# Kernel optimization log

Measured on AMD Instinct MI355X. Metric: run time of the kernel, lower is better.

Reference implementation:

```python
import jax, jax.numpy as jnp
import numpy as np

K = 128      # num_states
V = 50257    # vocab_size
D = 128      # tag_emb_dim
H = 128      # trans_hidden_dim
B = 64       # batch
T = 2048     # seq len


def setup_inputs() -> dict:
    key = jax.random.key(0)
    ks = jax.random.split(key, 6)
    s = 0.02
    return {
        "batch_emissions": jax.random.randint(ks[0], (B, T), 0, V, dtype=jnp.int32),
        "init_logits": jnp.zeros((K,), jnp.float32),
        "tag_embed": (jax.random.normal(ks[1], (K, D)) * s).astype(jnp.float32),
        "word_embed": (jax.random.normal(ks[2], (V, D)) * s).astype(jnp.float32),
        "word_bias": jnp.zeros((V,), jnp.float32),
        "trans_query": (jax.random.normal(ks[3], (H,)) * s).astype(jnp.float32),
        "trans_W": (jax.random.normal(ks[4], (K * K, H)) * s).astype(jnp.float32),
        "trans_b": jnp.zeros((K * K,), jnp.float32),
    }


def reference(batch_emissions, init_logits, tag_embed, word_embed, word_bias,
              trans_query, trans_W, trans_b):
    # log initial probs (K,)
    log_pi = jax.nn.log_softmax(init_logits)
    # log transition probs (K, K): row i = p(z_t | z_{t-1}=i)
    log_A = jax.nn.log_softmax((trans_W @ trans_query + trans_b).reshape(K, K), axis=1)
    # log emission probs (K, V)
    log_Bm = jax.nn.log_softmax(tag_embed @ word_embed.T + word_bias[None, :], axis=1)
    # gather per-token emissions: (B, T, K)
    emit = log_Bm.T[batch_emissions]

    alpha0 = log_pi[None, :] + emit[:, 0]  # (B, K)

    def step(alpha, e_t):
        # alpha: (B, K) over prev state i; log-semiring matvec with log_A
        a = jax.scipy.special.logsumexp(alpha[:, :, None] + log_A[None, :, :], axis=1) + e_t
        return a, None

    emit_rest = jnp.swapaxes(emit[:, 1:], 0, 1)  # (T-1, B, K)
    alpha_T, _ = jax.lax.scan(step, alpha0, emit_rest)

    log_likelihood = jax.scipy.special.logsumexp(alpha_T, axis=-1)  # (B,)
    return -jnp.sum(log_likelihood)
```

## Files before the change

### kernel.cpp

```cpp
#include <hip/hip_runtime.h>


#define KK 128
#define TT 2048
#define BB 64

typedef int v8i __attribute__((ext_vector_type(8)));
typedef float v4f __attribute__((ext_vector_type(4)));

__device__ __forceinline__ float wave_sum64(float v) {
#pragma unroll
  for (int m = 32; m; m >>= 1) v += __shfl_xor(v, m, 64);
  return v;
}
__device__ __forceinline__ float wave_max64(float v) {
#pragma unroll
  for (int m = 32; m; m >>= 1) v = fmaxf(v, __shfl_xor(v, m, 64));
  return v;
}
__device__ __forceinline__ unsigned short f2bf(float x) {
  union { float f; unsigned u; } c; c.f = x;
  unsigned r = c.u + 0x7fffu + ((c.u >> 16) & 1u);
  return (unsigned short)(r >> 16);
}
__device__ __forceinline__ float bflo(unsigned u) {
  union { unsigned u; float f; } c; c.u = u << 16; return c.f;
}
__device__ __forceinline__ float bfhi(unsigned u) {
  union { unsigned u; float f; } c; c.u = u & 0xffff0000u; return c.f;
}

__device__ __forceinline__ float fp8dec_sw(unsigned byte) {
  unsigned em = byte & 0x7fu;
  float v;
  if (em < 8) {
    v = (float)em * 0x1p-9f;
  } else {
    union { unsigned u; float f; } x;
    x.u = (em << 20) + (120u << 23);
    v = x.f;
  }
  return (byte & 0x80u) ? -v : v;
}

__global__ __launch_bounds__(128, 1)
void k_emis(const float* __restrict__ tag, const float* __restrict__ word,
            const float* __restrict__ bias, unsigned short* __restrict__ E128,
            float* __restrict__ partialZ, int V) {
  __shared__ float4 wtile[128 * 32];
  __shared__ float btile[128];
  const int tid = threadIdx.x;
  const int v0 = blockIdx.x * 128;

  const float4* w4 = (const float4*)word;
  const int maxi = V * 32 - 1;
#pragma unroll
  for (int it = 0; it < 32; ++it) {
    int idx = it * 128 + tid;
    int g = v0 * 32 + idx;
    wtile[idx] = w4[min(g, maxi)];
  }
  btile[tid] = (v0 + tid < V) ? bias[v0 + tid] : 0.f;

  float treg[128];
  const float4* t4 = (const float4*)(tag + (size_t)tid * 128);
#pragma unroll
  for (int c = 0; c < 32; ++c) {
    float4 x = t4[c];
    treg[4 * c + 0] = x.x; treg[4 * c + 1] = x.y;
    treg[4 * c + 2] = x.z; treg[4 * c + 3] = x.w;
  }
  __syncthreads();

  float zp = 0.f;
  for (int v = 0; v < 128; ++v) {
    if (v0 + v >= V) break;
    const float4* row = &wtile[v * 32];
    float a0 = 0.f, a1 = 0.f, a2 = 0.f, a3 = 0.f;
#pragma unroll
    for (int c = 0; c < 32; ++c) {
      float4 pv = row[c];
      a0 = fmaf(pv.x, treg[4 * c + 0], a0);
      a1 = fmaf(pv.y, treg[4 * c + 1], a1);
      a2 = fmaf(pv.z, treg[4 * c + 2], a2);
      a3 = fmaf(pv.w, treg[4 * c + 3], a3);
    }
    float e = __expf((a0 + a1) + (a2 + a3) + btile[v]);
    E128[(size_t)(v0 + v) * KK + tid] = f2bf(128.f * e);
    zp += e;
  }
  partialZ[(size_t)blockIdx.x * KK + tid] = zp;
}

__global__ __launch_bounds__(128)
void k_trans(const float* __restrict__ W, const float* __restrict__ q,
             const float* __restrict__ tb, const float* __restrict__ pZ,
             const float* __restrict__ initlog, float* __restrict__ A2,
             float* __restrict__ A2p, float* __restrict__ piZ,
             float* __restrict__ piPlain, float* __restrict__ Zinv,
             int nPart, int V) {
  __shared__ float qs[KK];
  __shared__ float r0[2], r1[2];
  const int j = threadIdx.x, i = blockIdx.x;
  qs[j] = q[j];
  __syncthreads();

  const float4* w4 = (const float4*)(W + ((size_t)(i * KK + j)) * KK);
  const float4* q4 = (const float4*)qs;
  float a0 = 0.f, a1 = 0.f, a2 = 0.f, a3 = 0.f;
#pragma unroll
  for (int c = 0; c < KK / 4; ++c) {
    float4 wv = w4[c], qv = q4[c];
    a0 = fmaf(wv.x, qv.x, a0); a1 = fmaf(wv.y, qv.y, a1);
    a2 = fmaf(wv.z, qv.z, a2); a3 = fmaf(wv.w, qv.w, a3);
  }
  float logit = (a0 + a1) + (a2 + a3) + tb[i * KK + j];

  float m = wave_max64(logit);
  if ((j & 63) == 0) r0[j >> 6] = m;
  __syncthreads();
  m = fmaxf(r0[0], r0[1]);
  float e = __expf(logit - m);
  float s = wave_sum64(e);
  if ((j & 63) == 0) r1[j >> 6] = s;
  __syncthreads();
  s = r1[0] + r1[1];

  float Z0 = 0.f, Z1 = 0.f, Z2 = 0.f, Z3 = 0.f;
  float Z4 = 0.f, Z5 = 0.f, Z6 = 0.f, Z7 = 0.f;
  int p = 0;
  for (; p + 8 <= nPart; p += 8) {
    Z0 += pZ[(size_t)(p + 0) * KK + j]; Z1 += pZ[(size_t)(p + 1) * KK + j];
    Z2 += pZ[(size_t)(p + 2) * KK + j]; Z3 += pZ[(size_t)(p + 3) * KK + j];
    Z4 += pZ[(size_t)(p + 4) * KK + j]; Z5 += pZ[(size_t)(p + 5) * KK + j];
    Z6 += pZ[(size_t)(p + 6) * KK + j]; Z7 += pZ[(size_t)(p + 7) * KK + j];
  }
  for (; p < nPart; ++p) Z0 += pZ[(size_t)p * KK + j];
  float Z = ((Z0 + Z1) + (Z2 + Z3)) + ((Z4 + Z5) + (Z6 + Z7));

  A2[i * KK + j] = e / (s * Z);
  A2p[i * KK + j] = 128.0f * e / s;

  if (i == 0) {
    float x = initlog[j];
    __syncthreads();
    float m2 = wave_max64(x);
    if ((j & 63) == 0) r0[j >> 6] = m2;
    __syncthreads();
    m2 = fmaxf(r0[0], r0[1]);
    float e2 = __expf(x - m2);
    float s2 = wave_sum64(e2);
    if ((j & 63) == 0) r1[j >> 6] = s2;
    __syncthreads();
    s2 = r1[0] + r1[1];
    piZ[j] = e2 / (s2 * Z);
    piPlain[j] = e2 / s2;
    Zinv[j] = (float)V / Z;
  }
}

__device__ __forceinline__ void scan_step(
    int n, int nst, const int* __restrict__ tks,
    const unsigned short* __restrict__ E128, const v8i (&af)[8], v8i (&Q)[8],
    uint2 (&evU)[8], uint2 (&evL)[8], int g) {
  v4f ev4[8];
#pragma unroll
  for (int it = 0; it < 8; ++it) {
    ev4[it][0] = bflo(evU[it].x); ev4[it][1] = bfhi(evU[it].x);
    ev4[it][2] = bflo(evU[it].y); ev4[it][3] = bfhi(evU[it].y);
  }
  int np = (n + 1 < nst) ? n + 1 : nst - 1;
  const unsigned short* ern = E128 + (size_t)tks[np] * KK;
#pragma unroll
  for (int it = 0; it < 8; ++it)
    evL[it] = *(const uint2*)(ern + 16 * it + 4 * g);

  const v4f ZED = {0.f, 0.f, 0.f, 0.f};
#pragma unroll
  for (int jt = 0; jt < 8; ++jt) {
    v4f acc[8];
#pragma unroll
    for (int it = 0; it < 8; ++it)
      acc[it] = __builtin_amdgcn_mfma_scale_f32_16x16x128_f8f6f4(
          af[it], Q[jt], ZED, 0, 0, 0, 0x78787878, 0, 0x78787878);
#pragma unroll
    for (int it = 0; it < 8; ++it) {
      v4f nn = acc[it] * ev4[it];
      int w = __builtin_amdgcn_cvt_pk_fp8_f32(nn[0], nn[1], 0, false);
      w = __builtin_amdgcn_cvt_pk_fp8_f32(nn[2], nn[3], w, true);
      Q[jt][it] = w;
    }
  }
}

template <int NS>
__global__ __launch_bounds__(64, 2)
void k_scan(const int* __restrict__ toks, const unsigned short* __restrict__ E128,
            const float* __restrict__ A2p, const float* __restrict__ Zinv,
            uint4* __restrict__ P) {
  __shared__ int tks[64];
  const int chain = blockIdx.x;
  const int s = chain >> 6;
  const int b = chain & 63;
  const int l = threadIdx.x, m = l & 15, g = l >> 4;
  const int t0 = 1 + (2047 * s) / NS;
  const int nst = (2047 * (s + 1)) / NS - (2047 * s) / NS;
  if (l < nst) tks[l] = toks[(size_t)b * TT + t0 + l];

  v8i af[8];
#pragma unroll
  for (int it = 0; it < 8; ++it) {
    const int colj = 16 * it + m;
    const float zj = Zinv[colj];
#pragma unroll
    for (int w = 0; w < 8; ++w) {
      const float* ap = A2p + (size_t)(16 * w + 4 * g) * KK + colj;
      int ww = __builtin_amdgcn_cvt_pk_fp8_f32(ap[0] * zj, ap[KK] * zj, 0, false);
      ww = __builtin_amdgcn_cvt_pk_fp8_f32(ap[2 * KK] * zj, ap[3 * KK] * zj, ww, true);
      af[it][w] = ww;
    }
  }

  v8i Q[8];
  const unsigned diag = (g == (m >> 2)) ? (0x70u << (8 * (m & 3))) : 0u;
#pragma unroll
  for (int jt = 0; jt < 8; ++jt) {
#pragma unroll
    for (int w = 0; w < 8; ++w) Q[jt][w] = (w == jt) ? (int)diag : 0;
  }

  __syncthreads();

  uint2 evA[8], evB[8];
  {
    const unsigned short* er0 = E128 + (size_t)tks[0] * KK;
#pragma unroll
    for (int it = 0; it < 8; ++it) evA[it] = *(const uint2*)(er0 + 16 * it + 4 * g);
  }
  const int pairs = nst >> 1;
  for (int c = 0; c < pairs; ++c) {
    scan_step(2 * c + 0, nst, tks, E128, af, Q, evA, evB, g);
    scan_step(2 * c + 1, nst, tks, E128, af, Q, evB, evA, g);
  }
  if (nst & 1) scan_step(nst - 1, nst, tks, E128, af, Q, evA, evB, g);

  uint4* base = P + (size_t)chain * 1024;
#pragma unroll
  for (int jt = 0; jt < 8; ++jt) {
    union { v8i v; uint4 u[2]; } x; x.v = Q[jt];
    base[jt * 128 + l * 2 + 0] = x.u[0];
    base[jt * 128 + l * 2 + 1] = x.u[1];
  }
}

__global__ __launch_bounds__(256, 1)
void k_comb(const uint4* __restrict__ P, const float* __restrict__ piPlain,
            const unsigned short* __restrict__ E128, const float* __restrict__ Zinv,
            const int* __restrict__ toks, float* __restrict__ ll, int V,
            int nseg) {
  __shared__ float alpha[KK];
  const int b = blockIdx.x;
  const int tid = threadIdx.x;
  const int h = tid >> 6;
  const int l = tid & 63, m = l & 15, g = l >> 4;

  if (tid < KK) {
    int tok0 = toks[(size_t)b * TT];
    alpha[tid] = piPlain[tid] * bflo((unsigned)E128[(size_t)tok0 * KK + tid]) *
                 Zinv[tid];
  }
  __syncthreads();

  const unsigned* P32 = (const unsigned*)P;
  for (int s = 0; s < nseg; ++s) {
    const size_t cbase = ((size_t)(s * 64 + b)) * 4096;
    float ac[8];
#pragma unroll
    for (int jt = 0; jt < 8; ++jt) ac[jt] = alpha[16 * jt + m];
    float out[8];
#pragma unroll
    for (int k = 0; k < 8; ++k) out[k] = 0.f;
#pragma unroll
    for (int jt = 0; jt < 8; ++jt) {
      const float aj = ac[jt];
#pragma unroll
      for (int w2 = 0; w2 < 2; ++w2) {
        unsigned wd = P32[cbase + jt * 512 + l * 8 + (2 * h + w2)];
#if __has_builtin(__builtin_amdgcn_cvt_f32_fp8)
        out[w2 * 4 + 0] = fmaf(__builtin_amdgcn_cvt_f32_fp8((int)wd, 0), aj, out[w2 * 4 + 0]);
        out[w2 * 4 + 1] = fmaf(__builtin_amdgcn_cvt_f32_fp8((int)wd, 1), aj, out[w2 * 4 + 1]);
        out[w2 * 4 + 2] = fmaf(__builtin_amdgcn_cvt_f32_fp8((int)wd, 2), aj, out[w2 * 4 + 2]);
        out[w2 * 4 + 3] = fmaf(__builtin_amdgcn_cvt_f32_fp8((int)wd, 3), aj, out[w2 * 4 + 3]);
#else
#pragma unroll
        for (int c = 0; c < 4; ++c) {
          float v = fp8dec_sw((wd >> (8 * c)) & 0xffu);
          out[w2 * 4 + c] = fmaf(v, aj, out[w2 * 4 + c]);
        }
#endif
      }
    }
    __syncthreads();
#pragma unroll
    for (int k = 0; k < 8; ++k) {
      out[k] += __shfl_xor(out[k], 1, 64);
      out[k] += __shfl_xor(out[k], 2, 64);
      out[k] += __shfl_xor(out[k], 4, 64);
      out[k] += __shfl_xor(out[k], 8, 64);
    }
    if (m == 0) {
#pragma unroll
      for (int w2 = 0; w2 < 2; ++w2)
#pragma unroll
        for (int c = 0; c < 4; ++c)
          alpha[16 * (2 * h + w2) + 4 * g + c] =
              out[w2 * 4 + c] * 0.0078125f;
    }
    __syncthreads();
  }

  if (h == 0) {
    float sm = alpha[l] + alpha[l + 64];
    sm = wave_sum64(sm);
    const float C = (float)(log(128.0) + (double)TT * log((double)V));
    if (l == 0) ll[b] = __logf(sm) - C;
  }
}

__global__ __launch_bounds__(256, 1)
void k_fwd_fb(const int* __restrict__ toks, const unsigned short* __restrict__ E128,
              const float* __restrict__ A2, const float* __restrict__ piZ,
              float* __restrict__ ll) {
  __shared__ float pb[2][KK];
  __shared__ float part[2 * KK];
  __shared__ int tk[TT];
  __shared__ float red[4];
  const int tid = threadIdx.x;
  const int j = tid & (KK - 1);
  const int h = tid >> 7;
  const int b = blockIdx.x;

  const int4* t4 = (const int4*)(toks + (size_t)b * TT);
  int4* l4 = (int4*)tk;
#pragma unroll
  for (int c = 0; c < TT / 4 / 256; ++c) l4[c * 256 + tid] = t4[c * 256 + tid];

  float Areg[64];
  {
    const float* Acol = A2 + (size_t)(h * 64) * KK + j;
#pragma unroll
    for (int i = 0; i < 64; ++i) Areg[i] = Acol[i * KK];
  }
  __syncthreads();

  const unsigned short* Ej = E128 + j;
  const float inv128 = 0.0078125f;
  float eA = inv128 * bflo((unsigned)Ej[(size_t)tk[1] * KK]);
  float eB = inv128 * bflo((unsigned)Ej[(size_t)tk[2] * KK]);
  float eC = inv128 * bflo((unsigned)Ej[(size_t)tk[3] * KK]);
  float eD = inv128 * bflo((unsigned)Ej[(size_t)tk[4] * KK]);
  if (h == 0) pb[0][j] = piZ[j] * inv128 * bflo((unsigned)Ej[(size_t)tk[0] * KK]);
  float Lacc = 0.f;
  __syncthreads();

  for (int t = 1; t < TT; ++t) {
    const float4* ph = (const float4*)&pb[(t - 1) & 1][h * 64];
    float a0 = 0.f, a1 = 0.f, a2 = 0.f, a3 = 0.f;
#pragma unroll
    for (int c = 0; c < 16; ++c) {
      float4 pv = ph[c];
      a0 = fmaf(pv.x, Areg[4 * c + 0], a0);
      a1 = fmaf(pv.y, Areg[4 * c + 1], a1);
      a2 = fmaf(pv.z, Areg[4 * c + 2], a2);
      a3 = fmaf(pv.w, Areg[4 * c + 3], a3);
    }
    part[2 * j + h] = (a0 + a1) + (a2 + a3);
    __syncthreads();

    float e = eA; eA = eB; eB = eC; eC = eD;
    int tn = tk[t + 4 < TT ? t + 4 : TT - 1];
    eD = inv128 * bflo((unsigned)Ej[(size_t)tn * KK]);

    float np = 0.f;
    if (h == 0) {
      float2 pr = *(const float2*)&part[2 * j];
      np = (pr.x + pr.y) * e;
    }
    if ((t & 63) == 0) {
      float v = wave_sum64(np);
      if ((tid & 63) == 0) red[tid >> 6] = v;
      __syncthreads();
      float tot = (red[0] + red[1]) + (red[2] + red[3]);
      np *= __builtin_amdgcn_rcpf(tot);
      if (tid == 0) Lacc += __logf(tot);
    } else if ((t & 3) == 0) {
      np *= 0x1p64f;
    }
    if (h == 0) pb[t & 1][j] = np;
    __syncthreads();
  }

  float lv = (h == 0) ? pb[(TT - 1) & 1][j] : 0.f;
  float v = wave_sum64(lv);
  if ((tid & 63) == 0) red[tid >> 6] = v;
  __syncthreads();
  float tot = (red[0] + red[1]) + (red[2] + red[3]);
  const float RESCALE_C = (float)(30720.0 * 0.6931471805599453);
  if (tid == 0) ll[b] = Lacc + __logf(tot) - RESCALE_C;
}

__global__ void k_final(const float* __restrict__ ll, float* __restrict__ out) {
  float v = ll[threadIdx.x];
  v = wave_sum64(v);
  if (threadIdx.x == 0) out[0] = -v;
}

extern "C" void kernel_launch(void* const* d_in, const int* in_sizes, int n_in,
                              void* d_out, int out_size, void* d_ws, size_t ws_size,
                              hipStream_t stream) {
  const int*   toks    = (const int*)d_in[0];
  const float* initlog = (const float*)d_in[1];
  const float* tag     = (const float*)d_in[2];
  const float* word    = (const float*)d_in[3];
  const float* bias    = (const float*)d_in[4];
  const float* q       = (const float*)d_in[5];
  const float* W       = (const float*)d_in[6];
  const float* tb      = (const float*)d_in[7];
  float* out = (float*)d_out;

  const int V = in_sizes[4];
  const int nPart = (V + 127) / 128;

  unsigned short* E128 = (unsigned short*)d_ws;
  float* pZ      = (float*)(E128 + (size_t)V * KK);
  float* A2      = pZ + (size_t)nPart * KK;
  float* A2p     = A2 + KK * KK;
  float* piZ     = A2p + KK * KK;
  float* piPlain = piZ + KK;
  float* Zinv    = piPlain + KK;
  float* ll      = Zinv + KK;
  uintptr_t pp = (uintptr_t)(ll + BB);
  pp = (pp + 15) & ~(uintptr_t)15;
  uint4* P = (uint4*)pp;

  const size_t head = pp - (uintptr_t)d_ws;
  const size_t need32 = head + (size_t)32 * BB * 1024 * sizeof(uint4);

  k_emis <<<nPart, 128, 0, stream>>>(tag, word, bias, E128, pZ, V);
  k_trans<<<KK, 128, 0, stream>>>(W, q, tb, pZ, initlog, A2, A2p, piZ,
                                  piPlain, Zinv, nPart, V);
  if (ws_size >= need32) {
    k_scan<32><<<32 * BB, 64, 0, stream>>>(toks, E128, A2p, Zinv, P);
    k_comb<<<BB, 256, 0, stream>>>(P, piPlain, E128, Zinv, toks, ll, V, 32);
  } else {
    k_fwd_fb<<<BB, 256, 0, stream>>>(toks, E128, A2, piZ, ll);
  }
  k_final<<<1, BB, 0, stream>>>(ll, out);
}
```

Baseline: 374.3 us.

## Split scan transfer-matrix columns across four blocks and use fewer, longer segments

The scan kernel now gives each (segment, batch) chain's 128 output columns to four separate blocks, each holding 2 of the 8 column tiles of Q. The time dimension is cut into 12 segments instead of 32, so each block runs about 170 steps with a smaller register footprint, and the occupancy hint rises to 3 blocks per SIMD. The intent is to raise parallelism per chain and reduce the sequential combine work while keeping grid size similar. Each block now redoes the emission-row loads and the fp8 A setup on its own, and the per-step serial chain is longer.

```diff
diff --git a/kernel.cpp b/kernel.cpp
--- a/kernel.cpp
+++ b/kernel.cpp
@@ -159,16 +159,10 @@
   }
 }
 
-__device__ __forceinline__ void scan_step(
+__device__ __forceinline__ void scan_step_q(
     int n, int nst, const int* __restrict__ tks,
-    const unsigned short* __restrict__ E128, const v8i (&af)[8], v8i (&Q)[8],
+    const unsigned short* __restrict__ E128, const v8i (&af)[8], v8i (&Q)[2],
     uint2 (&evU)[8], uint2 (&evL)[8], int g) {
-  v4f ev4[8];
-#pragma unroll
-  for (int it = 0; it < 8; ++it) {
-    ev4[it][0] = bflo(evU[it].x); ev4[it][1] = bfhi(evU[it].x);
-    ev4[it][2] = bflo(evU[it].y); ev4[it][3] = bfhi(evU[it].y);
-  }
   int np = (n + 1 < nst) ? n + 1 : nst - 1;
   const unsigned short* ern = E128 + (size_t)tks[np] * KK;
 #pragma unroll
@@ -177,35 +171,39 @@
 
   const v4f ZED = {0.f, 0.f, 0.f, 0.f};
 #pragma unroll
-  for (int jt = 0; jt < 8; ++jt) {
+  for (int jtl = 0; jtl < 2; ++jtl) {
     v4f acc[8];
 #pragma unroll
     for (int it = 0; it < 8; ++it)
       acc[it] = __builtin_amdgcn_mfma_scale_f32_16x16x128_f8f6f4(
-          af[it], Q[jt], ZED, 0, 0, 0, 0x78787878, 0, 0x78787878);
+          af[it], Q[jtl], ZED, 0, 0, 0, 0x78787878, 0, 0x78787878);
 #pragma unroll
     for (int it = 0; it < 8; ++it) {
-      v4f nn = acc[it] * ev4[it];
+      v4f e;
+      e[0] = bflo(evU[it].x); e[1] = bfhi(evU[it].x);
+      e[2] = bflo(evU[it].y); e[3] = bfhi(evU[it].y);
+      v4f nn = acc[it] * e;
       int w = __builtin_amdgcn_cvt_pk_fp8_f32(nn[0], nn[1], 0, false);
       w = __builtin_amdgcn_cvt_pk_fp8_f32(nn[2], nn[3], w, true);
-      Q[jt][it] = w;
+      Q[jtl][it] = w;
     }
   }
 }
 
 template <int NS>
-__global__ __launch_bounds__(64, 2)
+__global__ __launch_bounds__(64, 3)
 void k_scan(const int* __restrict__ toks, const unsigned short* __restrict__ E128,
             const float* __restrict__ A2p, const float* __restrict__ Zinv,
             uint4* __restrict__ P) {
-  __shared__ int tks[64];
-  const int chain = blockIdx.x;
-  const int s = chain >> 6;
-  const int b = chain & 63;
+  __shared__ int tks[(2047 + NS - 1) / NS + 1];
+  const int bid = blockIdx.x;
+  const int s = bid >> 8;
+  const int qq = (bid >> 6) & 3;
+  const int b = bid & 63;
   const int l = threadIdx.x, m = l & 15, g = l >> 4;
   const int t0 = 1 + (2047 * s) / NS;
   const int nst = (2047 * (s + 1)) / NS - (2047 * s) / NS;
-  if (l < nst) tks[l] = toks[(size_t)b * TT + t0 + l];
+  for (int i = l; i < nst; i += 64) tks[i] = toks[(size_t)b * TT + t0 + i];
 
   v8i af[8];
 #pragma unroll
@@ -221,12 +219,13 @@
     }
   }
 
-  v8i Q[8];
+  v8i Q[2];
   const unsigned diag = (g == (m >> 2)) ? (0x70u << (8 * (m & 3))) : 0u;
 #pragma unroll
-  for (int jt = 0; jt < 8; ++jt) {
-#pragma unroll
-    for (int w = 0; w < 8; ++w) Q[jt][w] = (w == jt) ? (int)diag : 0;
+  for (int jtl = 0; jtl < 2; ++jtl) {
+    const int jtg = 2 * qq + jtl;
+#pragma unroll
+    for (int w = 0; w < 8; ++w) Q[jtl][w] = (w == jtg) ? (int)diag : 0;
   }
 
   __syncthreads();
@@ -239,17 +238,18 @@
   }
   const int pairs = nst >> 1;
   for (int c = 0; c < pairs; ++c) {
-    scan_step(2 * c + 0, nst, tks, E128, af, Q, evA, evB, g);
-    scan_step(2 * c + 1, nst, tks, E128, af, Q, evB, evA, g);
-  }
-  if (nst & 1) scan_step(nst - 1, nst, tks, E128, af, Q, evA, evB, g);
-
-  uint4* base = P + (size_t)chain * 1024;
-#pragma unroll
-  for (int jt = 0; jt < 8; ++jt) {
-    union { v8i v; uint4 u[2]; } x; x.v = Q[jt];
-    base[jt * 128 + l * 2 + 0] = x.u[0];
-    base[jt * 128 + l * 2 + 1] = x.u[1];
+    scan_step_q(2 * c + 0, nst, tks, E128, af, Q, evA, evB, g);
+    scan_step_q(2 * c + 1, nst, tks, E128, af, Q, evB, evA, g);
+  }
+  if (nst & 1) scan_step_q(nst - 1, nst, tks, E128, af, Q, evA, evB, g);
+
+  uint4* base = P + ((size_t)(s * 64 + b)) * 1024;
+#pragma unroll
+  for (int jtl = 0; jtl < 2; ++jtl) {
+    const int jtg = 2 * qq + jtl;
+    union { v8i v; uint4 u[2]; } x; x.v = Q[jtl];
+    base[jtg * 128 + l * 2 + 0] = x.u[0];
+    base[jtg * 128 + l * 2 + 1] = x.u[1];
   }
 }
 
@@ -444,14 +444,14 @@
   uint4* P = (uint4*)pp;
 
   const size_t head = pp - (uintptr_t)d_ws;
-  const size_t need32 = head + (size_t)32 * BB * 1024 * sizeof(uint4);
+  const size_t need12 = head + (size_t)12 * BB * 1024 * sizeof(uint4);
 
   k_emis <<<nPart, 128, 0, stream>>>(tag, word, bias, E128, pZ, V);
   k_trans<<<KK, 128, 0, stream>>>(W, q, tb, pZ, initlog, A2, A2p, piZ,
                                   piPlain, Zinv, nPart, V);
-  if (ws_size >= need32) {
-    k_scan<32><<<32 * BB, 64, 0, stream>>>(toks, E128, A2p, Zinv, P);
-    k_comb<<<BB, 256, 0, stream>>>(P, piPlain, E128, Zinv, toks, ll, V, 32);
+  if (ws_size >= need12) {
+    k_scan<12><<<12 * 4 * BB, 64, 0, stream>>>(toks, E128, A2p, Zinv, P);
+    k_comb<<<BB, 256, 0, stream>>>(P, piPlain, E128, Zinv, toks, ll, V, 12);
   } else {
     k_fwd_fb<<<BB, 256, 0, stream>>>(toks, E128, A2, piZ, ll);
   }
```

New measurement: 447.3 us. 1.2x slower.
